# Performance work log

Measured on AMD Instinct MI355X. Metric: run time of the kernel, lower is better.

Reference implementation:

```python
import jax, jax.numpy as jnp
import numpy as np

B, T, M, L_TP = 32, 4096, 256, 128


def setup_inputs() -> dict:
    key = jax.random.key(0)
    k1, k2, k3, k4 = jax.random.split(key, 4)
    h_1 = jax.random.normal(k1, (B, T, M), dtype=jnp.float32)
    h_2 = jax.random.normal(k2, (B, T, M), dtype=jnp.float32)
    # trunc_normal(mean=-0.1, std=0.1) approximated by clipped normal
    w_tp = jnp.clip(-0.1 + 0.1 * jax.random.normal(k3, (1, L_TP), dtype=jnp.float32), -0.3, 0.1)
    v_tp = jnp.clip(-0.1 + 0.1 * jax.random.normal(k4, (L_TP, M), dtype=jnp.float32), -0.3, 0.1)
    return {"h_1": h_1, "h_2": h_2, "w_tp": w_tp, "v_tp": v_tp}


def reference(h_1, h_2, w_tp, v_tp):
    # Batched over all T timesteps at once (original loops in Python).
    # h: (B, T, 2, M) -- the 2-way stack of the two streams per timestep
    h = jnp.stack([h_1, h_2], axis=2)
    # tanh MLP hidden: (B, T, 2, L_tp)
    temp = jnp.tanh(jnp.einsum('lm,btcm->btcl', v_tp, h))
    # attention logits: (B, T, 2); softmax over the 2-way axis
    scores = jnp.einsum('l,btcl->btc', w_tp[0], temp)
    A = jax.nn.softmax(scores, axis=2)
    # original returns permute of concat (T, 2, B) -> (B, 2, T)
    return jnp.transpose(A, (0, 2, 1))
```

## Files before the change

kernel.cpp:

```cpp
#include <hip/hip_runtime.h>


typedef unsigned short u16;
typedef unsigned int   u32;
typedef __bf16 bf16x8 __attribute__((ext_vector_type(8)));
typedef float  f32x4  __attribute__((ext_vector_type(4)));

union ABFrag { bf16x8 v; u16 u[8]; uint4 q4; };

__device__ __forceinline__ u16 f2bf(float f) {
  u32 u = __float_as_uint(f);
  u += 0x7fffu + ((u >> 16) & 1u);
  return (u16)(u >> 16);
}

__device__ __forceinline__ float fast_tanh(float x) {
  float t = __builtin_amdgcn_exp2f(2.885390082f * x);
  return 1.0f - 2.0f * __builtin_amdgcn_rcpf(t + 1.0f);
}

#define NWG     512
#define ITERS   4
#define VSTRIDE 264

__global__ __launch_bounds__(512, 4) void topo_attn_kernel(
    const float* __restrict__ h1, const float* __restrict__ h2,
    const float* __restrict__ w,  const float* __restrict__ vfp,
    float* __restrict__ out) {
  __shared__ __align__(16) u16 vlds[128 * VSTRIDE];

  const int tid = threadIdx.x;

  {
    const float4* src = (const float4*)vfp;
    #pragma unroll
    for (int k = 0; k < 8; ++k) {
      int gi = k * 512 + tid;
      float4 f0 = src[gi * 2];
      float4 f1 = src[gi * 2 + 1];
      ABFrag t;
      t.u[0] = f2bf(f0.x); t.u[1] = f2bf(f0.y); t.u[2] = f2bf(f0.z); t.u[3] = f2bf(f0.w);
      t.u[4] = f2bf(f1.x); t.u[5] = f2bf(f1.y); t.u[6] = f2bf(f1.z); t.u[7] = f2bf(f1.w);
      int l = gi >> 5;
      int g = gi & 31;
      *(uint4*)&vlds[l * VSTRIDE + g * 8] = t.q4;
    }
  }
  __syncthreads();

  const int lane = tid & 63;
  const int wave = tid >> 6;
  const int l15  = lane & 15;
  const int q    = lane >> 4;

  float wreg[8];
  #pragma unroll
  for (int lt = 0; lt < 8; ++lt) wreg[lt] = w[lt * 16 + l15];

  const int row8 = l15 & 7;
  const float* hbase = (l15 < 8) ? h1 : h2;
  const int n0base = blockIdx.x * 64 + wave * 8;
  const float4* p = (const float4*)(hbase + (size_t)(n0base + row8) * 256) + q * 2;

  int vbase[8];
  #pragma unroll
  for (int lt = 0; lt < 8; ++lt)
    vbase[lt] = ((lt * 16 + l15) * VSTRIDE + q * 8) * 2;

  float4 bufA[3], bufB[3];
  bufA[0] = p[0]; bufB[0] = p[1];
  bufA[1] = p[8]; bufB[1] = p[9];

  #pragma unroll
  for (int it = 0; it < ITERS; ++it) {
    f32x4 acc[8];
    #pragma unroll
    for (int lt = 0; lt < 8; ++lt) acc[lt] = (f32x4){0.f, 0.f, 0.f, 0.f};

    #pragma unroll
    for (int ks = 0; ks < 8; ++ks) {
      const int s = it * 8 + ks;
      if (s + 2 < ITERS * 8) {
        const int s2  = s + 2;
        const int it2 = s2 >> 3, ks2 = s2 & 7;
        const float4* pp = p + it2 * 2097152 + ks2 * 8;
        bufA[s2 % 3] = pp[0];
        bufB[s2 % 3] = pp[1];
      }
      float4 fa = bufA[s % 3], fb = bufB[s % 3];
      ABFrag a;
      a.u[0] = f2bf(fa.x); a.u[1] = f2bf(fa.y); a.u[2] = f2bf(fa.z); a.u[3] = f2bf(fa.w);
      a.u[4] = f2bf(fb.x); a.u[5] = f2bf(fb.y); a.u[6] = f2bf(fb.z); a.u[7] = f2bf(fb.w);
      #pragma unroll
      for (int lt = 0; lt < 8; ++lt) {
        bf16x8 bfr = *(const bf16x8*)((const char*)vlds + (vbase[lt] + ks * 64));
        acc[lt] = __builtin_amdgcn_mfma_f32_16x16x32_bf16(a.v, bfr, acc[lt], 0, 0, 0);
      }
    }

    float s_p[4] = {0.f, 0.f, 0.f, 0.f};
    #pragma unroll
    for (int lt = 0; lt < 8; ++lt) {
      #pragma unroll
      for (int r = 0; r < 4; ++r)
        s_p[r] += wreg[lt] * fast_tanh(acc[lt][r]);
    }
    #pragma unroll
    for (int r = 0; r < 4; ++r) {
      #pragma unroll
      for (int off = 1; off < 16; off <<= 1)
        s_p[r] += __shfl_xor(s_p[r], off);
    }
    const int r = l15 & 3;
    float sel = (r == 0) ? s_p[0] : (r == 1) ? s_p[1] : (r == 2) ? s_p[2] : s_p[3];
    float oth = __shfl_xor(sel, 32);
    if (q < 2 && l15 < 4) {
      int n = n0base + it * 32768 + q * 4 + l15;
      int b = n >> 12, t = n & 4095;
      float e  = __builtin_amdgcn_exp2f(-1.442695041f * (sel - oth));
      float a0 = __builtin_amdgcn_rcpf(1.0f + e);
      out[b * 8192 + t]        = a0;
      out[b * 8192 + 4096 + t] = 1.0f - a0;
    }
  }
}

extern "C" void kernel_launch(void* const* d_in, const int* in_sizes, int n_in,
                              void* d_out, int out_size, void* d_ws, size_t ws_size,
                              hipStream_t stream) {
  const float* h1 = (const float*)d_in[0];
  const float* h2 = (const float*)d_in[1];
  const float* w  = (const float*)d_in[2];
  const float* v  = (const float*)d_in[3];
  float* out = (float*)d_out;

  topo_attn_kernel<<<NWG, 512, 0, stream>>>(h1, h2, w, v, out);
}
```

Baseline: 287.5 us.

## Stream activations via global_load_lds DMA into swizzled LDS ring buffers

Activation rows are now copied from global memory directly into a per-wave triple-buffered LDS ring with global_load_lds, and explicit vmcnt waits replace the register prefetch. The V matrix LDS layout moves from padded rows to an XOR-style rotation swizzle to avoid bank conflicts. Workgroup count is halved, each group runs twice as many iterations, and occupancy drops to 2 blocks per CU because dynamic shared memory grows. The aim is to cut VGPR pressure and use wider coalesced loads, at the cost of lower occupancy and an extra LDS round-trip.

Measured after the change: 281.2 us. 1.02x faster.

```diff
diff --git a/kernel.cpp b/kernel.cpp
--- a/kernel.cpp
+++ b/kernel.cpp
@@ -19,15 +19,26 @@
   return 1.0f - 2.0f * __builtin_amdgcn_rcpf(t + 1.0f);
 }
 
-#define NWG     512
-#define ITERS   4
-#define VSTRIDE 264
+typedef const __attribute__((address_space(1))) void gvoid;
+typedef __attribute__((address_space(3))) void lvoid;
 
-__global__ __launch_bounds__(512, 4) void topo_attn_kernel(
+__device__ __forceinline__ void dma16(const char* g, char* l) {
+  __builtin_amdgcn_global_load_lds((gvoid*)g, (lvoid*)l, 16, 0, 0);
+}
+
+#define NWG    256
+#define ITERS  8
+#define TOT    (ITERS * 8)
+#define ITSTR  (NWG * 64 * 1024)
+#define SMEMSZ (65536 + 8 * 3 * 2048)
+
+__global__ __launch_bounds__(512, 2) void topo_attn_kernel(
     const float* __restrict__ h1, const float* __restrict__ h2,
     const float* __restrict__ w,  const float* __restrict__ vfp,
     float* __restrict__ out) {
-  __shared__ __align__(16) u16 vlds[128 * VSTRIDE];
+  extern __shared__ __align__(16) char smem[];
+  u16*  vlds   = (u16*)smem;
+  char* albase = smem + 65536;
 
   const int tid = threadIdx.x;
 
@@ -43,7 +54,7 @@
       t.u[4] = f2bf(f1.x); t.u[5] = f2bf(f1.y); t.u[6] = f2bf(f1.z); t.u[7] = f2bf(f1.w);
       int l = gi >> 5;
       int g = gi & 31;
-      *(uint4*)&vlds[l * VSTRIDE + g * 8] = t.q4;
+      *(uint4*)&vlds[(l << 8) + (((g + l) & 31) << 3)] = t.q4;
     }
   }
   __syncthreads();
@@ -57,19 +68,25 @@
   #pragma unroll
   for (int lt = 0; lt < 8; ++lt) wreg[lt] = w[lt * 16 + l15];
 
-  const int row8 = l15 & 7;
-  const float* hbase = (l15 < 8) ? h1 : h2;
-  const int n0base = blockIdx.x * 64 + wave * 8;
-  const float4* p = (const float4*)(hbase + (size_t)(n0base + row8) * 256) + q * 2;
+  char* aslot = albase + wave * 6144;
 
-  int vbase[8];
-  #pragma unroll
-  for (int lt = 0; lt < 8; ++lt)
-    vbase[lt] = ((lt * 16 + l15) * VSTRIDE + q * 8) * 2;
+  const int rr = lane >> 3;
+  const int cc = lane & 7;
+  const int gchunk = (cc - rr) & 7;
 
-  float4 bufA[3], bufB[3];
-  bufA[0] = p[0]; bufB[0] = p[1];
-  bufA[1] = p[8]; bufB[1] = p[9];
+  const int n0base = (blockIdx.x * 8 + wave) * 8;
+  const char* g1 = (const char*)h1 + (size_t)(n0base + rr) * 1024 + gchunk * 16;
+  const char* g2 = (const char*)h2 + (size_t)(n0base + rr) * 1024 + gchunk * 16;
+
+  const int r7 = l15 & 7;
+  const int fragbase = (l15 >> 3) * 1024 + r7 * 128;
+  const int j1 = ((2 * q + r7) & 7) * 16;
+  const int j2 = ((2 * q + 1 + r7) & 7) * 16;
+
+  {
+    dma16(g1, aslot);            dma16(g2, aslot + 1024);
+    dma16(g1 + 128, aslot + 2048); dma16(g2 + 128, aslot + 2048 + 1024);
+  }
 
   #pragma unroll
   for (int it = 0; it < ITERS; ++it) {
@@ -80,20 +97,27 @@
     #pragma unroll
     for (int ks = 0; ks < 8; ++ks) {
       const int s = it * 8 + ks;
-      if (s + 2 < ITERS * 8) {
-        const int s2  = s + 2;
-        const int it2 = s2 >> 3, ks2 = s2 & 7;
-        const float4* pp = p + it2 * 2097152 + ks2 * 8;
-        bufA[s2 % 3] = pp[0];
-        bufB[s2 % 3] = pp[1];
+      if (s + 2 < TOT) {
+        const int s2 = s + 2;
+        const size_t off = (size_t)(s2 >> 3) * ITSTR + (s2 & 7) * 128;
+        char* dst = aslot + (s2 % 3) * 2048;
+        dma16(g1 + off, dst);
+        dma16(g2 + off, dst + 1024);
       }
-      float4 fa = bufA[s % 3], fb = bufB[s % 3];
+      if (s + 2 < TOT)      asm volatile("s_waitcnt vmcnt(4)" ::: "memory");
+      else if (s + 1 < TOT) asm volatile("s_waitcnt vmcnt(2)" ::: "memory");
+      else                  asm volatile("s_waitcnt vmcnt(0)" ::: "memory");
+
+      const char* ab = aslot + (s % 3) * 2048 + fragbase;
+      float4 fa = *(const float4*)(ab + j1);
+      float4 fb = *(const float4*)(ab + j2);
       ABFrag a;
       a.u[0] = f2bf(fa.x); a.u[1] = f2bf(fa.y); a.u[2] = f2bf(fa.z); a.u[3] = f2bf(fa.w);
       a.u[4] = f2bf(fb.x); a.u[5] = f2bf(fb.y); a.u[6] = f2bf(fb.z); a.u[7] = f2bf(fb.w);
       #pragma unroll
       for (int lt = 0; lt < 8; ++lt) {
-        bf16x8 bfr = *(const bf16x8*)((const char*)vlds + (vbase[lt] + ks * 64));
+        const int l = (lt << 4) + l15;
+        bf16x8 bfr = *(const bf16x8*)&vlds[(l << 8) + (((4 * ks + q + l) & 31) << 3)];
         acc[lt] = __builtin_amdgcn_mfma_f32_16x16x32_bf16(a.v, bfr, acc[lt], 0, 0, 0);
       }
     }
@@ -115,7 +139,7 @@
     float sel = (r == 0) ? s_p[0] : (r == 1) ? s_p[1] : (r == 2) ? s_p[2] : s_p[3];
     float oth = __shfl_xor(sel, 32);
     if (q < 2 && l15 < 4) {
-      int n = n0base + it * 32768 + q * 4 + l15;
+      int n = n0base + it * (NWG * 64) + q * 4 + l15;
       int b = n >> 12, t = n & 4095;
       float e  = __builtin_amdgcn_exp2f(-1.442695041f * (sel - oth));
       float a0 = __builtin_amdgcn_rcpf(1.0f + e);
@@ -134,5 +158,9 @@
   const float* v  = (const float*)d_in[3];
   float* out = (float*)d_out;
 
-  topo_attn_kernel<<<NWG, 512, 0, stream>>>(h1, h2, w, v, out);
+  static int attr_set = 0;
+  (void)attr_set;
+  hipFuncSetAttribute((const void*)topo_attn_kernel,
+                      hipFuncAttributeMaxDynamicSharedMemorySize, SMEMSZ);
+  topo_attn_kernel<<<NWG, 512, SMEMSZ, stream>>>(h1, h2, w, v, out);
 }
```
